# Optimization experiments

Hardware: AMD Instinct MI355X
Metric: run time of the kernel (lower is better)

The kernel has to match this reference:

```python
import jax, jax.numpy as jnp
import numpy as np

B, OBS, H, A, E = 131072, 194, 64, 5, 3  # batch, obs dim, hidden, max_action_dim, n event types


def setup_inputs() -> dict:
    key = jax.random.key(0)
    ks = jax.random.split(key, 16)
    s = lambda k, shape, std=0.1: (jax.random.normal(k, shape, dtype=jnp.float32) * std)
    return {
        "x": jax.random.normal(ks[0], (B, OBS), dtype=jnp.float32),
        "action": jax.random.randint(ks[1], (B,), 0, A),
        "W1": s(ks[2], (OBS, H)), "b1": jnp.zeros((H,), jnp.float32),
        "W2": s(ks[3], (H, H)),   "b2": jnp.zeros((H,), jnp.float32),
        "Wh": s(ks[4], (E, H, A), 0.01), "bh": jnp.zeros((E, A), jnp.float32),
        "Wc1": s(ks[5], (OBS, H)), "bc1": jnp.zeros((H,), jnp.float32),
        "Wc2": s(ks[6], (H, H)),   "bc2": jnp.zeros((H,), jnp.float32),
        "Wc3": s(ks[7], (H, 1)),   "bc3": jnp.zeros((1,), jnp.float32),
    }


def reference(x, action, W1, b1, W2, b2, Wh, bh, Wc1, bc1, Wc2, bc2, Wc3, bc3):
    # shared trunk
    feat = jnp.tanh(jnp.tanh(x @ W1 + b1) @ W2 + b2)          # [B, H]
    # route each sample to one of E heads via argmax of first 3 obs dims
    ev = jnp.argmax(x[:, :E], axis=1)                          # [B] int
    all_logits = jnp.einsum('bh,eha->bea', feat, Wh) + bh      # [B, E, A]
    logits = jnp.take_along_axis(
        all_logits, jnp.broadcast_to(ev[:, None, None], (x.shape[0], 1, A)), axis=1
    )[:, 0]                                                    # [B, A]
    logp_all = jax.nn.log_softmax(logits, axis=-1)             # [B, A]
    logp = jnp.take_along_axis(logp_all, action[:, None], axis=1)[:, 0]  # [B]
    entropy = -jnp.sum(jnp.exp(logp_all) * logp_all, axis=-1)  # [B]
    # critic
    value = jnp.tanh(jnp.tanh(x @ Wc1 + bc1) @ Wc2 + bc2) @ Wc3 + bc3    # [B, 1]
    return action, logp, entropy, value
```

## Files before the change

### kernel.cpp

```cpp
#include <hip/hip_runtime.h>
#include <hip/hip_bf16.h>

constexpr int Bt    = 131072;
constexpr int OBS   = 194;

constexpr int W1B_S  = 0;
constexpr int WC1B_S = 14336;
constexpr int W2B_S  = 28672;
constexpr int WC2B_S = 36864;
constexpr int WHB_S  = 45056;

typedef short bf8   __attribute__((ext_vector_type(8)));
typedef float f32x4 __attribute__((ext_vector_type(4)));
typedef unsigned int u32;

__device__ __forceinline__ short f2bs(float f) {
    union { __hip_bfloat16 h; short s; } u;
    u.h = __float2bfloat16(f);
    return u.s;
}
__device__ __forceinline__ float bs2f(short s) {
    union { short s; __hip_bfloat16 h; } u;
    u.s = s;
    return __bfloat162float(u.h);
}
__device__ __forceinline__ u32 pk2(float a, float b) {
    union { __hip_bfloat162 h; u32 u; } r;
    r.h = __float22bfloat162_rn(float2{a, b});
    return r.u;
}
__device__ __forceinline__ float fast_tanh(float v) {
    v = fminf(fmaxf(v, -15.f), 15.f);
    float e = __expf(2.f * v);
    return (e - 1.f) * __builtin_amdgcn_rcpf(e + 1.f);
}
__device__ __forceinline__ void dma16(const void* g, void* s) {
    __builtin_amdgcn_global_load_lds(
        (const __attribute__((address_space(1))) u32*)g,
        (__attribute__((address_space(3))) u32*)s, 16, 0, 0);
}

__global__ void __launch_bounds__(256) prep(
    const float* __restrict__ W1, const float* __restrict__ b1,
    const float* __restrict__ W2, const float* __restrict__ Wh,
    const float* __restrict__ Wc1, const float* __restrict__ bc1,
    const float* __restrict__ Wc2, const float* __restrict__ Wc3,
    short* __restrict__ ws)
{
    const int gid = blockIdx.x * 256 + threadIdx.x;
    const int gsz = gridDim.x * 256;

    for (int i = gid; i < 14336; i += gsz) {
        int j = i & 7, l = (i >> 3) & 63, nt = (i >> 9) & 3, kb = i >> 11;
        int k = kb * 32 + ((l >> 4) << 3) + j;
        int n = nt * 16 + (l & 15);
        short v1 = 0, v2 = 0;
        if (k < OBS) {
            v1 = f2bs(W1[k * 64 + n]);
            v2 = f2bs(Wc1[k * 64 + n]);
        } else if (k == OBS) {
            v1 = f2bs(b1[n]);
            v2 = f2bs(bc1[n]);
        }
        ws[W1B_S + i]  = v1;
        ws[WC1B_S + i] = v2;
    }
    for (int i = gid; i < 8192; i += gsz) {
        int j = i & 7, l = (i >> 3) & 63, nt = (i >> 9) & 3, kb = i >> 11;
        int s = kb * 32 + ((l >> 4) << 3) + j;
        int kp = (s & 3) * 16 + (s >> 2);
        int n = nt * 16 + (l & 15);
        ws[W2B_S + i]  = f2bs(W2[kp * 64 + n]);
        ws[WC2B_S + i] = f2bs(Wc2[kp * 64 + n]);
    }
    for (int i = gid; i < 1024; i += gsz) {
        int j = i & 7, l = (i >> 3) & 63, kb = i >> 9;
        int s = kb * 32 + ((l >> 4) << 3) + j;
        int kp = (s & 3) * 16 + (s >> 2);
        int cc = l & 15;
        float v;
        if (cc == 15) v = Wc3[kp];
        else { int e = cc / 5, a = cc - 5 * e; v = Wh[(e * 64 + kp) * 5 + a]; }
        ws[WHB_S + i] = f2bs(v);
    }
}

constexpr int FB_LDS = 57344 + 8 * 2304;

__global__ void __launch_bounds__(512, 2) fused_ac(
    const float* __restrict__ x, const int* __restrict__ act_in,
    const float* __restrict__ b2, const float* __restrict__ bc2,
    const float* __restrict__ bh, const float* __restrict__ bc3,
    const short* __restrict__ ws,
    float* __restrict__ out)
{
    __shared__ __align__(16) char smem[FB_LDS];
    const int t = threadIdx.x;
    const int l = t & 63, q = (t >> 4) & 3, c = t & 15;
    const int wu = __builtin_amdgcn_readfirstlane(t >> 6);

    #pragma unroll
    for (int i = 0; i < 7; ++i) {
        int ch = wu * 7 + i;
        dma16((const char*)ws + ch * 1024 + l * 16, smem + ch * 1024);
    }

    const bf8* fW1L  = reinterpret_cast<const bf8*>(smem);
    const bf8* fWc1L = reinterpret_cast<const bf8*>(smem + 28672);
    short* bb = reinterpret_cast<short*>(smem + 57344 + wu * 2304);

    const int tt = blockIdx.x * 8 + wu;
    const float* xr = x + (size_t)tt * 16 * OBS + (size_t)c * OBS;

    union AF { u32 u[4]; bf8 v; } af[7];
    float4 f40;
    #pragma unroll
    for (int kb = 0; kb < 6; ++kb) {
        float4 a = *reinterpret_cast<const float4*>(xr + kb * 32 + q * 8);
        float4 b = *reinterpret_cast<const float4*>(xr + kb * 32 + q * 8 + 4);
        if (kb == 0) f40 = a;
        af[kb].u[0] = pk2(a.x, a.y);
        af[kb].u[1] = pk2(a.z, a.w);
        af[kb].u[2] = pk2(b.x, b.y);
        af[kb].u[3] = pk2(b.z, b.w);
    }
    af[6].u[0] = 0; af[6].u[1] = 0; af[6].u[2] = 0; af[6].u[3] = 0;
    if (q == 0) {
        float2 v = *reinterpret_cast<const float2*>(xr + 192);
        af[6].u[0] = pk2(v.x, v.y);
        af[6].u[1] = pk2(1.0f, 0.0f);
    }

    int act = 0, evc = 0;
    if (l < 16) {
        act = act_in[tt * 16 + l];
        float b = f40.x;
        if (f40.y > b) { b = f40.y; evc = 1; }
        if (f40.z > b) evc = 2;
    }

    float b2v[4], bc2v[4];
    #pragma unroll
    for (int nt = 0; nt < 4; ++nt) {
        b2v[nt]  = b2[nt * 16 + c];
        bc2v[nt] = bc2[nt * 16 + c];
    }
    float bhv = (c < 15) ? bh[c] : bc3[0];

    __syncthreads();

    f32x4 aa[4], ac[4];
    #pragma unroll
    for (int nt = 0; nt < 4; ++nt) {
        aa[nt] = f32x4{0.f, 0.f, 0.f, 0.f};
        ac[nt] = f32x4{0.f, 0.f, 0.f, 0.f};
    }
    #pragma unroll
    for (int kb = 0; kb < 7; ++kb) {
        bf8 a = af[kb].v;
        #pragma unroll
        for (int nt = 0; nt < 4; ++nt) {
            aa[nt] = __builtin_amdgcn_mfma_f32_16x16x32_bf16(a, fW1L [(kb * 4 + nt) * 64 + l], aa[nt], 0, 0, 0);
            ac[nt] = __builtin_amdgcn_mfma_f32_16x16x32_bf16(a, fWc1L[(kb * 4 + nt) * 64 + l], ac[nt], 0, 0, 0);
        }
    }

    auto bounce = [&](f32x4* cc4, bf8* fr) {
        #pragma unroll
        for (int r = 0; r < 4; ++r) {
            uint2 p;
            p.x = pk2(fast_tanh(cc4[0][r]), fast_tanh(cc4[1][r]));
            p.y = pk2(fast_tanh(cc4[2][r]), fast_tanh(cc4[3][r]));
            *reinterpret_cast<uint2*>(&bb[(q * 4 + r) * 72 + 4 * c]) = p;
        }
        #pragma unroll
        for (int kb = 0; kb < 2; ++kb)
            fr[kb] = *reinterpret_cast<const bf8*>(&bb[c * 72 + kb * 32 + q * 8]);
    };

    bf8 xa[2], xc[2];
    bounce(aa, xa);
    bounce(ac, xc);

    const bf8* fW2G  = reinterpret_cast<const bf8*>((const char*)ws + 57344);
    const bf8* fWc2G = reinterpret_cast<const bf8*>((const char*)ws + 73728);
    const bf8* fWhG  = reinterpret_cast<const bf8*>((const char*)ws + 90112);
    #pragma unroll
    for (int nt = 0; nt < 4; ++nt) {
        aa[nt] = f32x4{b2v[nt], b2v[nt], b2v[nt], b2v[nt]};
        ac[nt] = f32x4{bc2v[nt], bc2v[nt], bc2v[nt], bc2v[nt]};
    }
    #pragma unroll
    for (int kb = 0; kb < 2; ++kb) {
        #pragma unroll
        for (int nt = 0; nt < 4; ++nt) {
            aa[nt] = __builtin_amdgcn_mfma_f32_16x16x32_bf16(xa[kb], fW2G [(kb * 4 + nt) * 64 + l], aa[nt], 0, 0, 0);
            ac[nt] = __builtin_amdgcn_mfma_f32_16x16x32_bf16(xc[kb], fWc2G[(kb * 4 + nt) * 64 + l], ac[nt], 0, 0, 0);
        }
    }

    bf8 fa[2], fc[2];
    bounce(aa, fa);
    bounce(ac, fc);

    f32x4 lg = f32x4{bhv, bhv, bhv, bhv};
    f32x4 vv = f32x4{bhv, bhv, bhv, bhv};
    #pragma unroll
    for (int kb = 0; kb < 2; ++kb) {
        bf8 bw = fWhG[kb * 64 + l];
        lg = __builtin_amdgcn_mfma_f32_16x16x32_bf16(fa[kb], bw, lg, 0, 0, 0);
        vv = __builtin_amdgcn_mfma_f32_16x16x32_bf16(fc[kb], bw, vv, 0, 0, 0);
    }

    short* lw = bb;
    float* vb = reinterpret_cast<float*>(bb + 1120);
    #pragma unroll
    for (int r = 0; r < 4; ++r)
        lw[(q * 4 + r) * 18 + c] = f2bs(lg[r]);
    if (c == 15) {
        #pragma unroll
        for (int r = 0; r < 4; ++r)
            vb[q * 4 + r] = vv[r];
    }

    if (l < 16) {
        float lgv[5];
        #pragma unroll
        for (int a = 0; a < 5; ++a)
            lgv[a] = bs2f(lw[c * 18 + evc * 5 + a]);
        float mx = lgv[0];
        #pragma unroll
        for (int a = 1; a < 5; ++a) mx = fmaxf(mx, lgv[a]);
        float se = 0.f;
        #pragma unroll
        for (int a = 0; a < 5; ++a) se += __expf(lgv[a] - mx);
        float lse = __logf(se) + mx;
        float lsel = lgv[0];
        #pragma unroll
        for (int a = 1; a < 5; ++a) lsel = (act == a) ? lgv[a] : lsel;
        float ent = 0.f;
        #pragma unroll
        for (int a = 0; a < 5; ++a) { float lp = lgv[a] - lse; ent -= __expf(lp) * lp; }

        const int gm = tt * 16 + c;
        out[gm]          = (float)act;
        out[Bt + gm]     = lsel - lse;
        out[2 * Bt + gm] = ent;
        out[3 * Bt + gm] = vb[c];
    }
}

extern "C" void kernel_launch(void* const* d_in, const int* in_sizes, int n_in,
                              void* d_out, int out_size, void* d_ws, size_t ws_size,
                              hipStream_t stream) {
    const float* x   = (const float*)d_in[0];
    const int*   act = (const int*)  d_in[1];
    const float* W1  = (const float*)d_in[2];
    const float* b1  = (const float*)d_in[3];
    const float* W2  = (const float*)d_in[4];
    const float* b2  = (const float*)d_in[5];
    const float* Wh  = (const float*)d_in[6];
    const float* bh  = (const float*)d_in[7];
    const float* Wc1 = (const float*)d_in[8];
    const float* bc1 = (const float*)d_in[9];
    const float* Wc2 = (const float*)d_in[10];
    const float* bc2 = (const float*)d_in[11];
    const float* Wc3 = (const float*)d_in[12];
    const float* bc3 = (const float*)d_in[13];
    float* out = (float*)d_out;
    short* ws  = (short*)d_ws;

    hipLaunchKernelGGL(prep, dim3(32), dim3(256), 0, stream,
                       W1, b1, W2, Wh, Wc1, bc1, Wc2, Wc3, ws);
    hipLaunchKernelGGL(fused_ac, dim3(1024), dim3(512), 0, stream,
                       x, act, b2, bc2, bh, bc3, ws, out);
}
```

Baseline: 185.0 us.

## Process two row tiles per wave and prefetch second tile's inputs during compute

Each wave now handles two 16-row tiles, with half the blocks launched, so the LDS weight staging of W1/Wc1 is amortised over twice the rows. The second tile's x loads are issued in two halves, each placed behind a scheduling barrier before the first tile's layer-1 MFMAs and back-half compute, so global memory latency overlaps with matrix work. The cost is higher register pressure from holding the prefetched float4s, which may lower occupancy, and fewer blocks to spread across the CUs.

```diff
diff --git a/kernel.cpp b/kernel.cpp
--- a/kernel.cpp
+++ b/kernel.cpp
@@ -109,35 +109,10 @@
     const bf8* fWc1L = reinterpret_cast<const bf8*>(smem + 28672);
     short* bb = reinterpret_cast<short*>(smem + 57344 + wu * 2304);
 
-    const int tt = blockIdx.x * 8 + wu;
-    const float* xr = x + (size_t)tt * 16 * OBS + (size_t)c * OBS;
-
-    union AF { u32 u[4]; bf8 v; } af[7];
-    float4 f40;
-    #pragma unroll
-    for (int kb = 0; kb < 6; ++kb) {
-        float4 a = *reinterpret_cast<const float4*>(xr + kb * 32 + q * 8);
-        float4 b = *reinterpret_cast<const float4*>(xr + kb * 32 + q * 8 + 4);
-        if (kb == 0) f40 = a;
-        af[kb].u[0] = pk2(a.x, a.y);
-        af[kb].u[1] = pk2(a.z, a.w);
-        af[kb].u[2] = pk2(b.x, b.y);
-        af[kb].u[3] = pk2(b.z, b.w);
-    }
-    af[6].u[0] = 0; af[6].u[1] = 0; af[6].u[2] = 0; af[6].u[3] = 0;
-    if (q == 0) {
-        float2 v = *reinterpret_cast<const float2*>(xr + 192);
-        af[6].u[0] = pk2(v.x, v.y);
-        af[6].u[1] = pk2(1.0f, 0.0f);
-    }
-
-    int act = 0, evc = 0;
-    if (l < 16) {
-        act = act_in[tt * 16 + l];
-        float b = f40.x;
-        if (f40.y > b) { b = f40.y; evc = 1; }
-        if (f40.z > b) evc = 2;
-    }
+    const int tA = blockIdx.x * 16 + wu * 2;
+    const int tB = tA + 1;
+    const float* xrA = x + (size_t)tA * 16 * OBS + (size_t)c * OBS;
+    const float* xrB = x + (size_t)tB * 16 * OBS + (size_t)c * OBS;
 
     float b2v[4], bc2v[4];
     #pragma unroll
@@ -147,23 +122,51 @@
     }
     float bhv = (c < 15) ? bh[c] : bc3[0];
 
-    __syncthreads();
+    union AF { u32 u[4]; bf8 v; } afA[7], afB[7];
+    float4 f40A;
+    #pragma unroll
+    for (int kb = 0; kb < 6; ++kb) {
+        float4 a = *reinterpret_cast<const float4*>(xrA + kb * 32 + q * 8);
+        float4 b = *reinterpret_cast<const float4*>(xrA + kb * 32 + q * 8 + 4);
+        if (kb == 0) f40A = a;
+        afA[kb].u[0] = pk2(a.x, a.y);
+        afA[kb].u[1] = pk2(a.z, a.w);
+        afA[kb].u[2] = pk2(b.x, b.y);
+        afA[kb].u[3] = pk2(b.z, b.w);
+    }
+    afA[6].u[0] = 0; afA[6].u[1] = 0; afA[6].u[2] = 0; afA[6].u[3] = 0;
+    if (q == 0) {
+        float2 v = *reinterpret_cast<const float2*>(xrA + 192);
+        afA[6].u[0] = pk2(v.x, v.y);
+        afA[6].u[1] = pk2(1.0f, 0.0f);
+    }
+    int actA = 0, evA = 0, actB = 0, evB = 0;
+    if (l < 16) {
+        actA = act_in[tA * 16 + l];
+        actB = act_in[tB * 16 + l];
+        float bsa = f40A.x;
+        if (f40A.y > bsa) { bsa = f40A.y; evA = 1; }
+        if (f40A.z > bsa) evA = 2;
+    }
 
     f32x4 aa[4], ac[4];
-    #pragma unroll
-    for (int nt = 0; nt < 4; ++nt) {
-        aa[nt] = f32x4{0.f, 0.f, 0.f, 0.f};
-        ac[nt] = f32x4{0.f, 0.f, 0.f, 0.f};
-    }
-    #pragma unroll
-    for (int kb = 0; kb < 7; ++kb) {
-        bf8 a = af[kb].v;
+
+    auto layer1 = [&](union AF* af) {
         #pragma unroll
         for (int nt = 0; nt < 4; ++nt) {
-            aa[nt] = __builtin_amdgcn_mfma_f32_16x16x32_bf16(a, fW1L [(kb * 4 + nt) * 64 + l], aa[nt], 0, 0, 0);
-            ac[nt] = __builtin_amdgcn_mfma_f32_16x16x32_bf16(a, fWc1L[(kb * 4 + nt) * 64 + l], ac[nt], 0, 0, 0);
-        }
-    }
+            aa[nt] = f32x4{0.f, 0.f, 0.f, 0.f};
+            ac[nt] = f32x4{0.f, 0.f, 0.f, 0.f};
+        }
+        #pragma unroll
+        for (int kb = 0; kb < 7; ++kb) {
+            bf8 a = af[kb].v;
+            #pragma unroll
+            for (int nt = 0; nt < 4; ++nt) {
+                aa[nt] = __builtin_amdgcn_mfma_f32_16x16x32_bf16(a, fW1L [(kb * 4 + nt) * 64 + l], aa[nt], 0, 0, 0);
+                ac[nt] = __builtin_amdgcn_mfma_f32_16x16x32_bf16(a, fWc1L[(kb * 4 + nt) * 64 + l], ac[nt], 0, 0, 0);
+            }
+        }
+    };
 
     auto bounce = [&](f32x4* cc4, bf8* fr) {
         #pragma unroll
@@ -178,76 +181,128 @@
             fr[kb] = *reinterpret_cast<const bf8*>(&bb[c * 72 + kb * 32 + q * 8]);
     };
 
-    bf8 xa[2], xc[2];
-    bounce(aa, xa);
-    bounce(ac, xc);
-
     const bf8* fW2G  = reinterpret_cast<const bf8*>((const char*)ws + 57344);
     const bf8* fWc2G = reinterpret_cast<const bf8*>((const char*)ws + 73728);
     const bf8* fWhG  = reinterpret_cast<const bf8*>((const char*)ws + 90112);
-    #pragma unroll
-    for (int nt = 0; nt < 4; ++nt) {
-        aa[nt] = f32x4{b2v[nt], b2v[nt], b2v[nt], b2v[nt]};
-        ac[nt] = f32x4{bc2v[nt], bc2v[nt], bc2v[nt], bc2v[nt]};
-    }
-    #pragma unroll
-    for (int kb = 0; kb < 2; ++kb) {
+
+    auto backhalf = [&](int act, int evc, int tt) {
+        bf8 xa[2], xc[2];
+        bounce(aa, xa);
+        bounce(ac, xc);
         #pragma unroll
         for (int nt = 0; nt < 4; ++nt) {
-            aa[nt] = __builtin_amdgcn_mfma_f32_16x16x32_bf16(xa[kb], fW2G [(kb * 4 + nt) * 64 + l], aa[nt], 0, 0, 0);
-            ac[nt] = __builtin_amdgcn_mfma_f32_16x16x32_bf16(xc[kb], fWc2G[(kb * 4 + nt) * 64 + l], ac[nt], 0, 0, 0);
-        }
-    }
-
-    bf8 fa[2], fc[2];
-    bounce(aa, fa);
-    bounce(ac, fc);
-
-    f32x4 lg = f32x4{bhv, bhv, bhv, bhv};
-    f32x4 vv = f32x4{bhv, bhv, bhv, bhv};
-    #pragma unroll
-    for (int kb = 0; kb < 2; ++kb) {
-        bf8 bw = fWhG[kb * 64 + l];
-        lg = __builtin_amdgcn_mfma_f32_16x16x32_bf16(fa[kb], bw, lg, 0, 0, 0);
-        vv = __builtin_amdgcn_mfma_f32_16x16x32_bf16(fc[kb], bw, vv, 0, 0, 0);
-    }
-
-    short* lw = bb;
-    float* vb = reinterpret_cast<float*>(bb + 1120);
-    #pragma unroll
-    for (int r = 0; r < 4; ++r)
-        lw[(q * 4 + r) * 18 + c] = f2bs(lg[r]);
-    if (c == 15) {
+            aa[nt] = f32x4{b2v[nt], b2v[nt], b2v[nt], b2v[nt]};
+            ac[nt] = f32x4{bc2v[nt], bc2v[nt], bc2v[nt], bc2v[nt]};
+        }
+        #pragma unroll
+        for (int kb = 0; kb < 2; ++kb) {
+            #pragma unroll
+            for (int nt = 0; nt < 4; ++nt) {
+                aa[nt] = __builtin_amdgcn_mfma_f32_16x16x32_bf16(xa[kb], fW2G [(kb * 4 + nt) * 64 + l], aa[nt], 0, 0, 0);
+                ac[nt] = __builtin_amdgcn_mfma_f32_16x16x32_bf16(xc[kb], fWc2G[(kb * 4 + nt) * 64 + l], ac[nt], 0, 0, 0);
+            }
+        }
+        bf8 fa[2], fc[2];
+        bounce(aa, fa);
+        bounce(ac, fc);
+        f32x4 lg = f32x4{bhv, bhv, bhv, bhv};
+        f32x4 vv = f32x4{bhv, bhv, bhv, bhv};
+        #pragma unroll
+        for (int kb = 0; kb < 2; ++kb) {
+            bf8 bw = fWhG[kb * 64 + l];
+            lg = __builtin_amdgcn_mfma_f32_16x16x32_bf16(fa[kb], bw, lg, 0, 0, 0);
+            vv = __builtin_amdgcn_mfma_f32_16x16x32_bf16(fc[kb], bw, vv, 0, 0, 0);
+        }
+        short* lw = bb;
+        float* vb = reinterpret_cast<float*>(bb + 1120);
         #pragma unroll
         for (int r = 0; r < 4; ++r)
-            vb[q * 4 + r] = vv[r];
-    }
-
+            lw[(q * 4 + r) * 18 + c] = f2bs(lg[r]);
+        if (c == 15) {
+            #pragma unroll
+            for (int r = 0; r < 4; ++r)
+                vb[q * 4 + r] = vv[r];
+        }
+        if (l < 16) {
+            float lgv[5];
+            #pragma unroll
+            for (int a = 0; a < 5; ++a)
+                lgv[a] = bs2f(lw[c * 18 + evc * 5 + a]);
+            float mx = lgv[0];
+            #pragma unroll
+            for (int a = 1; a < 5; ++a) mx = fmaxf(mx, lgv[a]);
+            float se = 0.f;
+            #pragma unroll
+            for (int a = 0; a < 5; ++a) se += __expf(lgv[a] - mx);
+            float lse = __logf(se) + mx;
+            float lsel = lgv[0];
+            #pragma unroll
+            for (int a = 1; a < 5; ++a) lsel = (act == a) ? lgv[a] : lsel;
+            float ent = 0.f;
+            #pragma unroll
+            for (int a = 0; a < 5; ++a) { float lp = lgv[a] - lse; ent -= __expf(lp) * lp; }
+            const int gm = tt * 16 + c;
+            out[gm]          = (float)act;
+            out[Bt + gm]     = lsel - lse;
+            out[2 * Bt + gm] = ent;
+            out[3 * Bt + gm] = vb[c];
+        }
+    };
+
+    __syncthreads();
+
+    float4 rB0[6];
+    #pragma unroll
+    for (int kb = 0; kb < 3; ++kb) {
+        rB0[2 * kb]     = *reinterpret_cast<const float4*>(xrB + kb * 32 + q * 8);
+        rB0[2 * kb + 1] = *reinterpret_cast<const float4*>(xrB + kb * 32 + q * 8 + 4);
+    }
+    __builtin_amdgcn_sched_barrier(0);
+
+    layer1(afA);
+
+    #pragma unroll
+    for (int kb = 0; kb < 3; ++kb) {
+        float4 a = rB0[2 * kb], b = rB0[2 * kb + 1];
+        afB[kb].u[0] = pk2(a.x, a.y);
+        afB[kb].u[1] = pk2(a.z, a.w);
+        afB[kb].u[2] = pk2(b.x, b.y);
+        afB[kb].u[3] = pk2(b.z, b.w);
+    }
     if (l < 16) {
-        float lgv[5];
-        #pragma unroll
-        for (int a = 0; a < 5; ++a)
-            lgv[a] = bs2f(lw[c * 18 + evc * 5 + a]);
-        float mx = lgv[0];
-        #pragma unroll
-        for (int a = 1; a < 5; ++a) mx = fmaxf(mx, lgv[a]);
-        float se = 0.f;
-        #pragma unroll
-        for (int a = 0; a < 5; ++a) se += __expf(lgv[a] - mx);
-        float lse = __logf(se) + mx;
-        float lsel = lgv[0];
-        #pragma unroll
-        for (int a = 1; a < 5; ++a) lsel = (act == a) ? lgv[a] : lsel;
-        float ent = 0.f;
-        #pragma unroll
-        for (int a = 0; a < 5; ++a) { float lp = lgv[a] - lse; ent -= __expf(lp) * lp; }
-
-        const int gm = tt * 16 + c;
-        out[gm]          = (float)act;
-        out[Bt + gm]     = lsel - lse;
-        out[2 * Bt + gm] = ent;
-        out[3 * Bt + gm] = vb[c];
-    }
+        float4 f40B = rB0[0];
+        float bsb = f40B.x;
+        if (f40B.y > bsb) { bsb = f40B.y; evB = 1; }
+        if (f40B.z > bsb) evB = 2;
+    }
+    float4 rB1[6];
+    float2 t6B = float2{0.f, 0.f};
+    #pragma unroll
+    for (int kb = 3; kb < 6; ++kb) {
+        rB1[2 * (kb - 3)]     = *reinterpret_cast<const float4*>(xrB + kb * 32 + q * 8);
+        rB1[2 * (kb - 3) + 1] = *reinterpret_cast<const float4*>(xrB + kb * 32 + q * 8 + 4);
+    }
+    if (q == 0) t6B = *reinterpret_cast<const float2*>(xrB + 192);
+    __builtin_amdgcn_sched_barrier(0);
+
+    backhalf(actA, evA, tA);
+
+    #pragma unroll
+    for (int kb = 3; kb < 6; ++kb) {
+        float4 a = rB1[2 * (kb - 3)], b = rB1[2 * (kb - 3) + 1];
+        afB[kb].u[0] = pk2(a.x, a.y);
+        afB[kb].u[1] = pk2(a.z, a.w);
+        afB[kb].u[2] = pk2(b.x, b.y);
+        afB[kb].u[3] = pk2(b.z, b.w);
+    }
+    afB[6].u[0] = 0; afB[6].u[1] = 0; afB[6].u[2] = 0; afB[6].u[3] = 0;
+    if (q == 0) {
+        afB[6].u[0] = pk2(t6B.x, t6B.y);
+        afB[6].u[1] = pk2(1.0f, 0.0f);
+    }
+
+    layer1(afB);
+    backhalf(actB, evB, tB);
 }
 
 extern "C" void kernel_launch(void* const* d_in, const int* in_sizes, int n_in,
@@ -272,6 +327,6 @@
 
     hipLaunchKernelGGL(prep, dim3(32), dim3(256), 0, stream,
                        W1, b1, W2, Wh, Wc1, bc1, Wc2, Wc3, ws);
-    hipLaunchKernelGGL(fused_ac, dim3(1024), dim3(512), 0, stream,
+    hipLaunchKernelGGL(fused_ac, dim3(512), dim3(512), 0, stream,
                        x, act, b2, bc2, bh, bc3, ws, out);
 }
```

Result: slower. 192.7 us (+4.1%).

## Stage x tiles through LDS with coalesced loads, read weights from global

Applied to the files above, without the earlier changes.

Each wave now loads its contiguous 16-row x tile with fully coalesced 16-byte loads into a per-wave LDS buffer, then builds the MFMA A fragments from LDS. Previously each lane issued strided row loads straight from global. The layer-1 weights are no longer DMA'd into shared memory; they are read directly from global/L2. The block shrinks to 256 threads with more blocks and a changed occupancy hint. The aim is better global coalescing and higher occupancy, at the cost of repeated L2 reads of the weights and LDS bank-conflict risk from the 776-byte row stride.

```diff
diff --git a/kernel.cpp b/kernel.cpp
--- a/kernel.cpp
+++ b/kernel.cpp
@@ -33,11 +33,6 @@
     v = fminf(fmaxf(v, -15.f), 15.f);
     float e = __expf(2.f * v);
     return (e - 1.f) * __builtin_amdgcn_rcpf(e + 1.f);
-}
-__device__ __forceinline__ void dma16(const void* g, void* s) {
-    __builtin_amdgcn_global_load_lds(
-        (const __attribute__((address_space(1))) u32*)g,
-        (__attribute__((address_space(3))) u32*)s, 16, 0, 0);
 }
 
 __global__ void __launch_bounds__(256) prep(
@@ -85,9 +80,10 @@
     }
 }
 
-constexpr int FB_LDS = 57344 + 8 * 2304;
-
-__global__ void __launch_bounds__(512, 2) fused_ac(
+constexpr int XT_STR = 12544;
+constexpr int FB_LDS = 4 * XT_STR;
+
+__global__ void __launch_bounds__(256, 3) fused_ac(
     const float* __restrict__ x, const int* __restrict__ act_in,
     const float* __restrict__ b2, const float* __restrict__ bc2,
     const float* __restrict__ bh, const float* __restrict__ bc3,
@@ -99,34 +95,33 @@
     const int l = t & 63, q = (t >> 4) & 3, c = t & 15;
     const int wu = __builtin_amdgcn_readfirstlane(t >> 6);
 
-    #pragma unroll
-    for (int i = 0; i < 7; ++i) {
-        int ch = wu * 7 + i;
-        dma16((const char*)ws + ch * 1024 + l * 16, smem + ch * 1024);
-    }
-
-    const bf8* fW1L  = reinterpret_cast<const bf8*>(smem);
-    const bf8* fWc1L = reinterpret_cast<const bf8*>(smem + 28672);
-    short* bb = reinterpret_cast<short*>(smem + 57344 + wu * 2304);
-
-    const int tt = blockIdx.x * 8 + wu;
-    const float* xr = x + (size_t)tt * 16 * OBS + (size_t)c * OBS;
+    const int tt = blockIdx.x * 4 + wu;
+    const char* src = (const char*)x + (size_t)tt * 12416;
+    char* xs = smem + wu * XT_STR;
+
+    int4 stage[13];
+    #pragma unroll
+    for (int i = 0; i < 12; ++i)
+        stage[i] = *reinterpret_cast<const int4*>(src + i * 1024 + l * 16);
+    stage[12] = *reinterpret_cast<const int4*>(src + 11392 + l * 16);
+
+    #pragma unroll
+    for (int i = 0; i < 12; ++i)
+        *reinterpret_cast<int4*>(xs + i * 1024 + l * 16) = stage[i];
+    *reinterpret_cast<int4*>(xs + 11392 + l * 16) = stage[12];
 
     union AF { u32 u[4]; bf8 v; } af[7];
-    float4 f40;
     #pragma unroll
     for (int kb = 0; kb < 6; ++kb) {
-        float4 a = *reinterpret_cast<const float4*>(xr + kb * 32 + q * 8);
-        float4 b = *reinterpret_cast<const float4*>(xr + kb * 32 + q * 8 + 4);
-        if (kb == 0) f40 = a;
-        af[kb].u[0] = pk2(a.x, a.y);
-        af[kb].u[1] = pk2(a.z, a.w);
-        af[kb].u[2] = pk2(b.x, b.y);
-        af[kb].u[3] = pk2(b.z, b.w);
+        #pragma unroll
+        for (int j = 0; j < 4; ++j) {
+            float2 v = *reinterpret_cast<const float2*>(xs + c * 776 + kb * 128 + q * 32 + j * 8);
+            af[kb].u[j] = pk2(v.x, v.y);
+        }
     }
     af[6].u[0] = 0; af[6].u[1] = 0; af[6].u[2] = 0; af[6].u[3] = 0;
     if (q == 0) {
-        float2 v = *reinterpret_cast<const float2*>(xr + 192);
+        float2 v = *reinterpret_cast<const float2*>(xs + c * 776 + 768);
         af[6].u[0] = pk2(v.x, v.y);
         af[6].u[1] = pk2(1.0f, 0.0f);
     }
@@ -134,9 +129,11 @@
     int act = 0, evc = 0;
     if (l < 16) {
         act = act_in[tt * 16 + l];
-        float b = f40.x;
-        if (f40.y > b) { b = f40.y; evc = 1; }
-        if (f40.z > b) evc = 2;
+        float2 v01 = *reinterpret_cast<const float2*>(xs + l * 776);
+        float  v2  = *reinterpret_cast<const float*>(xs + l * 776 + 8);
+        float b = v01.x;
+        if (v01.y > b) { b = v01.y; evc = 1; }
+        if (v2 > b) evc = 2;
     }
 
     float b2v[4], bc2v[4];
@@ -147,7 +144,11 @@
     }
     float bhv = (c < 15) ? bh[c] : bc3[0];
 
-    __syncthreads();
+    const bf8* fW1G  = reinterpret_cast<const bf8*>((const char*)ws);
+    const bf8* fWc1G = reinterpret_cast<const bf8*>((const char*)ws + 28672);
+    const bf8* fW2G  = reinterpret_cast<const bf8*>((const char*)ws + 57344);
+    const bf8* fWc2G = reinterpret_cast<const bf8*>((const char*)ws + 73728);
+    const bf8* fWhG  = reinterpret_cast<const bf8*>((const char*)ws + 90112);
 
     f32x4 aa[4], ac[4];
     #pragma unroll
@@ -160,11 +161,12 @@
         bf8 a = af[kb].v;
         #pragma unroll
         for (int nt = 0; nt < 4; ++nt) {
-            aa[nt] = __builtin_amdgcn_mfma_f32_16x16x32_bf16(a, fW1L [(kb * 4 + nt) * 64 + l], aa[nt], 0, 0, 0);
-            ac[nt] = __builtin_amdgcn_mfma_f32_16x16x32_bf16(a, fWc1L[(kb * 4 + nt) * 64 + l], ac[nt], 0, 0, 0);
-        }
-    }
-
+            aa[nt] = __builtin_amdgcn_mfma_f32_16x16x32_bf16(a, fW1G [(kb * 4 + nt) * 64 + l], aa[nt], 0, 0, 0);
+            ac[nt] = __builtin_amdgcn_mfma_f32_16x16x32_bf16(a, fWc1G[(kb * 4 + nt) * 64 + l], ac[nt], 0, 0, 0);
+        }
+    }
+
+    short* bb = reinterpret_cast<short*>(xs);
     auto bounce = [&](f32x4* cc4, bf8* fr) {
         #pragma unroll
         for (int r = 0; r < 4; ++r) {
@@ -182,9 +184,6 @@
     bounce(aa, xa);
     bounce(ac, xc);
 
-    const bf8* fW2G  = reinterpret_cast<const bf8*>((const char*)ws + 57344);
-    const bf8* fWc2G = reinterpret_cast<const bf8*>((const char*)ws + 73728);
-    const bf8* fWhG  = reinterpret_cast<const bf8*>((const char*)ws + 90112);
     #pragma unroll
     for (int nt = 0; nt < 4; ++nt) {
         aa[nt] = f32x4{b2v[nt], b2v[nt], b2v[nt], b2v[nt]};
@@ -272,6 +271,6 @@
 
     hipLaunchKernelGGL(prep, dim3(32), dim3(256), 0, stream,
                        W1, b1, W2, Wh, Wc1, bc1, Wc2, Wc3, ws);
-    hipLaunchKernelGGL(fused_ac, dim3(1024), dim3(512), 0, stream,
+    hipLaunchKernelGGL(fused_ac, dim3(2048), dim3(256), 0, stream,
                        x, act, b2, bc2, bh, bc3, ws, out);
 }
```

Measured after the change: 192.1 us. 3.8% more time.
